# Kernel optimization log

Hardware: AMD Instinct MI355X
Metric: run time of the kernel (lower is better)

Reference implementation:

```python
import jax, jax.numpy as jnp
import numpy as np

Z_CH, TEXT_DIM, HID = 3, 512, 64
B, H, W = 16, 256, 256


def setup_inputs() -> dict:
    key = jax.random.key(0)
    ks = jax.random.split(key, 8)
    z = jax.random.normal(ks[0], (B, Z_CH, H, W), dtype=jnp.float32)
    text_vec = jax.random.normal(ks[1], (B, TEXT_DIM), dtype=jnp.float32)
    # 1x1 conv == per-pixel linear: store weights as [out, in]
    z_proj_w = jax.random.normal(ks[2], (HID, Z_CH), dtype=jnp.float32) * (1.0 / np.sqrt(Z_CH))
    z_proj_b = jnp.zeros((HID,), dtype=jnp.float32)
    text_proj_w = jax.random.normal(ks[3], (HID, TEXT_DIM), dtype=jnp.float32) * (1.0 / np.sqrt(TEXT_DIM))
    text_proj_b = jnp.zeros((HID,), dtype=jnp.float32)
    out_w = jax.random.normal(ks[4], (Z_CH, HID), dtype=jnp.float32) * (1.0 / np.sqrt(HID))
    out_b = jnp.zeros((Z_CH,), dtype=jnp.float32)
    log_gamma = jnp.asarray(1.0 / HID, dtype=jnp.float32)
    alpha = jnp.asarray(0.5, dtype=jnp.float32)
    c = jnp.asarray(1.0, dtype=jnp.float32)
    w = jnp.ones((3,), dtype=jnp.float32)
    return {"z": z, "text_vec": text_vec, "z_proj_w": z_proj_w, "z_proj_b": z_proj_b,
            "text_proj_w": text_proj_w, "text_proj_b": text_proj_b,
            "out_w": out_w, "out_b": out_b,
            "log_gamma": log_gamma, "alpha": alpha, "c": c, "w": w}


def reference(z, text_vec, z_proj_w, z_proj_b, text_proj_w, text_proj_b,
              out_w, out_b, log_gamma, alpha, c, w):
    # z_proj: 1x1 conv -> [B, HID, H, W]
    z_map = jnp.einsum('bchw,oc->bohw', z, z_proj_w) + z_proj_b[None, :, None, None]
    # text_proj: [B, HID]
    t = text_vec @ text_proj_w.T + text_proj_b
    # MultiKernel diagonal: k(z_i, t) per pixel. t_seq broadcasts the same
    # vector to all HW positions, so diag of the full [HW,HW] kernel matrix
    # equals the per-pixel kernel between z_map pixel and t.
    gamma = jnp.exp(log_gamma)
    diff = z_map - t[:, :, None, None]            # [B, HID, H, W]
    dist = jnp.sum(diff * diff, axis=1)            # squared euclidean, [B, H, W]
    k_lin = jnp.einsum('bchw,bc->bhw', z_map, t)   # [B, H, W]
    k_rbf = jnp.exp(-gamma * dist)
    k_poly = (alpha * k_lin + c) ** 2
    k = (w[0] * k_rbf + w[1] * k_lin + w[2] * k_poly) / (jnp.sum(w) + 1e-8)
    weight = k[:, None, :, :]                       # [B, 1, H, W]
    z_fused = z_map * (1.0 + jax.nn.sigmoid(weight))
    out = jnp.einsum('bchw,oc->bohw', z_fused, out_w) + out_b[None, :, None, None]
    return out
```

## Files before the change

kernel.cpp:

```cpp
#include <hip/hip_runtime.h>
#include <math.h>

#define HW_PIX 65536
#define TDIM 512

__device__ __forceinline__ float wred64(float v) {
#pragma unroll
    for (int off = 32; off > 0; off >>= 1) v += __shfl_xor(v, off, 64);
    return v;
}

__global__ __launch_bounds__(256) void fused_kernel(
    const float* __restrict__ z,
    const float* __restrict__ text_vec,
    const float* __restrict__ text_proj_w,
    const float* __restrict__ text_proj_b,
    const float* __restrict__ z_proj_w,
    const float* __restrict__ z_proj_b,
    const float* __restrict__ out_w,
    const float* __restrict__ out_bias,
    const float* __restrict__ log_gamma,
    const float* __restrict__ alpha_p,
    const float* __restrict__ c_p,
    const float* __restrict__ wv,
    float* __restrict__ out)
{
    const int blk = blockIdx.x;
    const int b   = blk >> 6;
    const int tid = threadIdx.x;

    __shared__ float t_sh[64];
    __shared__ float red[27];

    {
        const int o = tid >> 2;
        const int q = tid & 3;
        const float4* tv = (const float4*)(text_vec + (size_t)b * TDIM);
        const float4* wr = (const float4*)(text_proj_w + (size_t)o * TDIM);
        float acc = 0.f;
#pragma unroll 8
        for (int i = q * 32; i < q * 32 + 32; ++i) {
            float4 a = tv[i], w4 = wr[i];
            acc = fmaf(a.x, w4.x, fmaf(a.y, w4.y, fmaf(a.z, w4.z, fmaf(a.w, w4.w, acc))));
        }
        acc += __shfl_xor(acc, 1, 64);
        acc += __shfl_xor(acc, 2, 64);
        if (q == 0) t_sh[o] = acc + text_proj_b[o];
    }
    __syncthreads();

    {
        const int wave = tid >> 6, lane = tid & 63;
        const float t  = t_sh[lane];
        const float w0 = z_proj_w[lane * 3 + 0];
        const float w1 = z_proj_w[lane * 3 + 1];
        const float w2 = z_proj_w[lane * 3 + 2];
        const float zb = z_proj_b[lane];
        const float o0 = out_w[0 * 64 + lane];
        const float o1 = out_w[1 * 64 + lane];
        const float o2 = out_w[2 * 64 + lane];

        float pr[7];
        int n = 7;
        if (wave == 0) {
            pr[0] = w0 * t;  pr[1] = w1 * t;  pr[2] = w2 * t;
            pr[3] = zb * t;  pr[4] = t * t;   pr[5] = w0 * w0; pr[6] = w0 * w1;
        } else if (wave == 1) {
            pr[0] = w0 * w2; pr[1] = w1 * w1; pr[2] = w1 * w2;
            pr[3] = w2 * w2; pr[4] = o0 * w0; pr[5] = o0 * w1; pr[6] = o0 * w2;
        } else if (wave == 2) {
            pr[0] = o1 * w0; pr[1] = o1 * w1; pr[2] = o1 * w2;
            pr[3] = o2 * w0; pr[4] = o2 * w1; pr[5] = o2 * w2; pr[6] = o0 * zb;
        } else {
            pr[0] = o1 * zb; pr[1] = o2 * zb; pr[2] = w0 * zb;
            pr[3] = w1 * zb; pr[4] = w2 * zb; pr[5] = zb * zb; pr[6] = 0.f;
            n = 6;
        }
#pragma unroll
        for (int k = 0; k < 7; ++k) pr[k] = wred64(pr[k]);
        if (lane == 0) {
            const int base = wave * 7;
            for (int k = 0; k < n; ++k) red[base + k] = pr[k];
        }
    }
    __syncthreads();

    const float u0 = red[0], u1 = red[1], u2 = red[2], s = red[3], tn = red[4];
    const float G00 = red[5], G01 = red[6], G02 = red[7];
    const float G11 = red[8], G12 = red[9], G22 = red[10];
    const float M00 = red[11], M01 = red[12], M02 = red[13];
    const float M10 = red[14], M11 = red[15], M12 = red[16];
    const float M20 = red[17], M21 = red[18], M22 = red[19];
    const float v0 = red[20], v1 = red[21], v2 = red[22];
    const float g0 = red[23], g1 = red[24], g2 = red[25], bn = red[26];

    const float gamma = __expf(log_gamma[0]);
    const float alpha = alpha_p[0], cc = c_p[0];
    const float w0 = wv[0], w1 = wv[1], w2 = wv[2];
    const float invw = 1.0f / (w0 + w1 + w2 + 1e-8f);
    const float ob0 = out_bias[0], ob1 = out_bias[1], ob2 = out_bias[2];

    const float e0 = g0 - u0, e1 = g1 - u1, e2 = g2 - u2;
    const float d0 = bn - 2.f * s + tn;

    const int p = ((blk & 63) << 10) + (tid << 2);
    const float* zb = z + (size_t)b * 3 * HW_PIX + p;
    float4 q0 = *(const float4*)(zb);
    float4 q1 = *(const float4*)(zb + HW_PIX);
    float4 q2 = *(const float4*)(zb + 2 * HW_PIX);

    float X[4] = {q0.x, q0.y, q0.z, q0.w};
    float Y[4] = {q1.x, q1.y, q1.z, q1.w};
    float Z[4] = {q2.x, q2.y, q2.z, q2.w};
    float O0[4], O1[4], O2[4];

#pragma unroll
    for (int j = 0; j < 4; ++j) {
        const float x = X[j], y = Y[j], zc = Z[j];
        const float klin = fmaf(x, u0, fmaf(y, u1, fmaf(zc, u2, s)));
        const float quad = x * fmaf(2.f, fmaf(G01, y, G02 * zc), G00 * x)
                         + y * fmaf(2.f, G12 * zc, G11 * y)
                         + G22 * zc * zc;
        const float dist = quad + 2.f * fmaf(e0, x, fmaf(e1, y, e2 * zc)) + d0;
        const float krbf = __expf(-gamma * dist);
        float kp = fmaf(alpha, klin, cc);
        kp = kp * kp;
        const float k = (w0 * krbf + w1 * klin + w2 * kp) * invw;
        const float sig = 1.f / (1.f + __expf(-k));
        const float scale = 1.f + sig;

        const float m0 = fmaf(M00, x, fmaf(M01, y, fmaf(M02, zc, v0)));
        const float m1 = fmaf(M10, x, fmaf(M11, y, fmaf(M12, zc, v1)));
        const float m2 = fmaf(M20, x, fmaf(M21, y, fmaf(M22, zc, v2)));
        O0[j] = fmaf(scale, m0, ob0);
        O1[j] = fmaf(scale, m1, ob1);
        O2[j] = fmaf(scale, m2, ob2);
    }

    float* ob = out + (size_t)b * 3 * HW_PIX + p;
    *(float4*)(ob)              = make_float4(O0[0], O0[1], O0[2], O0[3]);
    *(float4*)(ob + HW_PIX)     = make_float4(O1[0], O1[1], O1[2], O1[3]);
    *(float4*)(ob + 2 * HW_PIX) = make_float4(O2[0], O2[1], O2[2], O2[3]);
}

extern "C" void kernel_launch(void* const* d_in, const int* in_sizes, int n_in,
                              void* d_out, int out_size, void* d_ws, size_t ws_size,
                              hipStream_t stream) {
    const float* z           = (const float*)d_in[0];
    const float* text_vec    = (const float*)d_in[1];
    const float* z_proj_w    = (const float*)d_in[2];
    const float* z_proj_b    = (const float*)d_in[3];
    const float* text_proj_w = (const float*)d_in[4];
    const float* text_proj_b = (const float*)d_in[5];
    const float* out_w       = (const float*)d_in[6];
    const float* out_b       = (const float*)d_in[7];
    const float* log_gamma   = (const float*)d_in[8];
    const float* alpha       = (const float*)d_in[9];
    const float* c           = (const float*)d_in[10];
    const float* w           = (const float*)d_in[11];
    float* out = (float*)d_out;
    (void)d_ws; (void)ws_size; (void)in_sizes; (void)n_in;

    fused_kernel<<<1024, 256, 0, stream>>>(z, text_vec, text_proj_w, text_proj_b,
                                           z_proj_w, z_proj_b, out_w, out_b,
                                           log_gamma, alpha, c, w, out);
}
```

Measured before the change: 115.5 us.

## Split constant precompute into prep kernel and widen streaming kernel to 8 pixels

The per-batch text projection and the weight Gram/product reductions, which every block used to recompute, move into a small 17-block prep kernel that writes the constants to workspace. The main kernel loads those constants as vectors, handles 8 pixels per thread over 512 blocks, and writes its output with nontemporal stores. This removes the redundant 512-wide dot products and block syncs from the streaming kernel. In exchange it adds a second kernel launch and a serial dependency through workspace, and halves the number of blocks.

Result: faster. 94.26 us (-18.4%).

```diff
diff --git a/kernel.cpp b/kernel.cpp
--- a/kernel.cpp
+++ b/kernel.cpp
@@ -3,6 +3,8 @@
 
 #define HW_PIX 65536
 #define TDIM 512
+
+typedef float f4 __attribute__((ext_vector_type(4)));
 
 __device__ __forceinline__ float wred64(float v) {
 #pragma unroll
@@ -10,8 +12,12 @@
     return v;
 }
 
-__global__ __launch_bounds__(256) void fused_kernel(
-    const float* __restrict__ z,
+__device__ __forceinline__ f4 ld4(const float* p) { return *(const f4*)p; }
+__device__ __forceinline__ void st4nt(float* p, f4 v) {
+    __builtin_nontemporal_store(v, (f4*)p);
+}
+
+__global__ __launch_bounds__(256) void prep_kernel(
     const float* __restrict__ text_vec,
     const float* __restrict__ text_proj_w,
     const float* __restrict__ text_proj_b,
@@ -23,16 +29,13 @@
     const float* __restrict__ alpha_p,
     const float* __restrict__ c_p,
     const float* __restrict__ wv,
-    float* __restrict__ out)
+    float* __restrict__ ws)
 {
     const int blk = blockIdx.x;
-    const int b   = blk >> 6;
     const int tid = threadIdx.x;
 
-    __shared__ float t_sh[64];
-    __shared__ float red[27];
-
-    {
+    if (blk < 16) {
+        const int b = blk;
         const int o = tid >> 2;
         const int q = tid & 3;
         const float4* tv = (const float4*)(text_vec + (size_t)b * TDIM);
@@ -45,13 +48,30 @@
         }
         acc += __shfl_xor(acc, 1, 64);
         acc += __shfl_xor(acc, 2, 64);
+
+        __shared__ float t_sh[64];
         if (q == 0) t_sh[o] = acc + text_proj_b[o];
-    }
-    __syncthreads();
-
-    {
+        __syncthreads();
+
+        if (tid < 64) {
+            const float t  = t_sh[tid];
+            const float w0 = z_proj_w[tid * 3 + 0];
+            const float w1 = z_proj_w[tid * 3 + 1];
+            const float w2 = z_proj_w[tid * 3 + 2];
+            const float zb = z_proj_b[tid];
+            float u0 = wred64(w0 * t);
+            float u1 = wred64(w1 * t);
+            float u2 = wred64(w2 * t);
+            float s  = wred64(zb * t);
+            float tn = wred64(t * t);
+            if (tid == 0) {
+                float* pb = ws + b * 8;
+                pb[0] = u0; pb[1] = u1; pb[2] = u2; pb[3] = s;
+                pb[4] = fmaf(-2.f, s, tn);
+            }
+        }
+    } else {
         const int wave = tid >> 6, lane = tid & 63;
-        const float t  = t_sh[lane];
         const float w0 = z_proj_w[lane * 3 + 0];
         const float w1 = z_proj_w[lane * 3 + 1];
         const float w2 = z_proj_w[lane * 3 + 2];
@@ -59,73 +79,90 @@
         const float o0 = out_w[0 * 64 + lane];
         const float o1 = out_w[1 * 64 + lane];
         const float o2 = out_w[2 * 64 + lane];
-
-        float pr[7];
-        int n = 7;
+        float* c = ws + 128;
         if (wave == 0) {
-            pr[0] = w0 * t;  pr[1] = w1 * t;  pr[2] = w2 * t;
-            pr[3] = zb * t;  pr[4] = t * t;   pr[5] = w0 * w0; pr[6] = w0 * w1;
+            float r0 = wred64(w0 * w0), r1 = wred64(w0 * w1), r2 = wred64(w0 * w2);
+            float r3 = wred64(w1 * w1), r4 = wred64(w1 * w2), r5 = wred64(w2 * w2);
+            if (lane == 0) { c[0]=r0; c[1]=r1; c[2]=r2; c[3]=r3; c[4]=r4; c[5]=r5; }
         } else if (wave == 1) {
-            pr[0] = w0 * w2; pr[1] = w1 * w1; pr[2] = w1 * w2;
-            pr[3] = w2 * w2; pr[4] = o0 * w0; pr[5] = o0 * w1; pr[6] = o0 * w2;
+            float r0 = wred64(o0 * w0), r1 = wred64(o0 * w1), r2 = wred64(o0 * w2);
+            float r3 = wred64(o1 * w0), r4 = wred64(o1 * w1), r5 = wred64(o1 * w2);
+            if (lane == 0) { c[6]=r0; c[7]=r1; c[8]=r2; c[9]=r3; c[10]=r4; c[11]=r5; }
         } else if (wave == 2) {
-            pr[0] = o1 * w0; pr[1] = o1 * w1; pr[2] = o1 * w2;
-            pr[3] = o2 * w0; pr[4] = o2 * w1; pr[5] = o2 * w2; pr[6] = o0 * zb;
+            float r0 = wred64(o2 * w0), r1 = wred64(o2 * w1), r2 = wred64(o2 * w2);
+            float r3 = wred64(zb * zb), r4 = wred64(o0 * zb), r5 = wred64(o1 * zb);
+            if (lane == 0) { c[12]=r0; c[13]=r1; c[14]=r2; c[15]=r3; c[16]=r4; c[17]=r5; }
         } else {
-            pr[0] = o1 * zb; pr[1] = o2 * zb; pr[2] = w0 * zb;
-            pr[3] = w1 * zb; pr[4] = w2 * zb; pr[5] = zb * zb; pr[6] = 0.f;
-            n = 6;
-        }
-#pragma unroll
-        for (int k = 0; k < 7; ++k) pr[k] = wred64(pr[k]);
-        if (lane == 0) {
-            const int base = wave * 7;
-            for (int k = 0; k < n; ++k) red[base + k] = pr[k];
+            float r0 = wred64(o2 * zb), r1 = wred64(w0 * zb);
+            float r2 = wred64(w1 * zb), r3 = wred64(w2 * zb);
+            if (lane == 0) {
+                c[18] = r0;
+                c[20] = r1; c[21] = r2; c[22] = r3;
+                c[19] = -__expf(log_gamma[0]);
+                c[23] = alpha_p[0];
+                c[24] = c_p[0];
+                float a = wv[0], bb = wv[1], d = wv[2];
+                float inv = 1.f / (a + bb + d + 1e-8f);
+                c[25] = a * inv; c[26] = bb * inv; c[27] = d * inv;
+                c[28] = out_bias[0]; c[29] = out_bias[1]; c[30] = out_bias[2];
+                c[31] = 0.f;
+            }
         }
     }
-    __syncthreads();
-
-    const float u0 = red[0], u1 = red[1], u2 = red[2], s = red[3], tn = red[4];
-    const float G00 = red[5], G01 = red[6], G02 = red[7];
-    const float G11 = red[8], G12 = red[9], G22 = red[10];
-    const float M00 = red[11], M01 = red[12], M02 = red[13];
-    const float M10 = red[14], M11 = red[15], M12 = red[16];
-    const float M20 = red[17], M21 = red[18], M22 = red[19];
-    const float v0 = red[20], v1 = red[21], v2 = red[22];
-    const float g0 = red[23], g1 = red[24], g2 = red[25], bn = red[26];
-
-    const float gamma = __expf(log_gamma[0]);
-    const float alpha = alpha_p[0], cc = c_p[0];
-    const float w0 = wv[0], w1 = wv[1], w2 = wv[2];
-    const float invw = 1.0f / (w0 + w1 + w2 + 1e-8f);
-    const float ob0 = out_bias[0], ob1 = out_bias[1], ob2 = out_bias[2];
-
+}
+
+__global__ __launch_bounds__(256) void fuse_kernel(
+    const float* __restrict__ z,
+    const float* __restrict__ ws,
+    float* __restrict__ out)
+{
+    const int blk = blockIdx.x;
+    const int b   = blk >> 5;
+    const int p   = ((blk & 31) << 11) + (threadIdx.x << 3);
+
+    const f4* C4 = (const f4*)(ws + 128);
+    const f4 f0 = C4[0], f1 = C4[1], f2 = C4[2], f3 = C4[3];
+    const f4 f4v = C4[4], f5 = C4[5], f6 = C4[6], f7 = C4[7];
+    const float G00=f0[0], G01=f0[1], G02=f0[2], G11=f0[3];
+    const float G12=f1[0], G22=f1[1], M00=f1[2], M01=f1[3];
+    const float M02=f2[0], M10=f2[1], M11=f2[2], M12=f2[3];
+    const float M20=f3[0], M21=f3[1], M22=f3[2], bn =f3[3];
+    const float v0=f4v[0], v1=f4v[1], v2=f4v[2], ngamma=f4v[3];
+    const float g0=f5[0], g1=f5[1], g2=f5[2], alpha=f5[3];
+    const float cc=f6[0], W0=f6[1], W1=f6[2], W2=f6[3];
+    const float ob0=f7[0], ob1=f7[1], ob2=f7[2];
+
+    const f4* pb4 = (const f4*)(ws + b * 8);
+    const f4 pbA = pb4[0], pbB = pb4[1];
+    const float u0=pbA[0], u1=pbA[1], u2=pbA[2], s=pbA[3];
+    const float d0 = bn + pbB[0];
     const float e0 = g0 - u0, e1 = g1 - u1, e2 = g2 - u2;
-    const float d0 = bn - 2.f * s + tn;
-
-    const int p = ((blk & 63) << 10) + (tid << 2);
+
     const float* zb = z + (size_t)b * 3 * HW_PIX + p;
-    float4 q0 = *(const float4*)(zb);
-    float4 q1 = *(const float4*)(zb + HW_PIX);
-    float4 q2 = *(const float4*)(zb + 2 * HW_PIX);
-
-    float X[4] = {q0.x, q0.y, q0.z, q0.w};
-    float Y[4] = {q1.x, q1.y, q1.z, q1.w};
-    float Z[4] = {q2.x, q2.y, q2.z, q2.w};
-    float O0[4], O1[4], O2[4];
-
+    f4 a0 = ld4(zb),            a1 = ld4(zb + 4);
+    f4 b0 = ld4(zb + HW_PIX),   b1 = ld4(zb + HW_PIX + 4);
+    f4 c0 = ld4(zb + 2*HW_PIX), c1 = ld4(zb + 2*HW_PIX + 4);
+
+    float X[8], Y[8], Z[8], O0[8], O1[8], O2[8];
 #pragma unroll
     for (int j = 0; j < 4; ++j) {
+        X[j] = a0[j]; X[j+4] = a1[j];
+        Y[j] = b0[j]; Y[j+4] = b1[j];
+        Z[j] = c0[j]; Z[j+4] = c1[j];
+    }
+
+#pragma unroll
+    for (int j = 0; j < 8; ++j) {
         const float x = X[j], y = Y[j], zc = Z[j];
         const float klin = fmaf(x, u0, fmaf(y, u1, fmaf(zc, u2, s)));
         const float quad = x * fmaf(2.f, fmaf(G01, y, G02 * zc), G00 * x)
                          + y * fmaf(2.f, G12 * zc, G11 * y)
                          + G22 * zc * zc;
         const float dist = quad + 2.f * fmaf(e0, x, fmaf(e1, y, e2 * zc)) + d0;
-        const float krbf = __expf(-gamma * dist);
+        const float krbf = __expf(ngamma * dist);
         float kp = fmaf(alpha, klin, cc);
         kp = kp * kp;
-        const float k = (w0 * krbf + w1 * klin + w2 * kp) * invw;
+        const float k = fmaf(W0, krbf, fmaf(W1, klin, W2 * kp));
         const float sig = 1.f / (1.f + __expf(-k));
         const float scale = 1.f + sig;
 
@@ -138,9 +175,13 @@
     }
 
     float* ob = out + (size_t)b * 3 * HW_PIX + p;
-    *(float4*)(ob)              = make_float4(O0[0], O0[1], O0[2], O0[3]);
-    *(float4*)(ob + HW_PIX)     = make_float4(O1[0], O1[1], O1[2], O1[3]);
-    *(float4*)(ob + 2 * HW_PIX) = make_float4(O2[0], O2[1], O2[2], O2[3]);
+    f4 r;
+    r[0]=O0[0]; r[1]=O0[1]; r[2]=O0[2]; r[3]=O0[3]; st4nt(ob, r);
+    r[0]=O0[4]; r[1]=O0[5]; r[2]=O0[6]; r[3]=O0[7]; st4nt(ob + 4, r);
+    r[0]=O1[0]; r[1]=O1[1]; r[2]=O1[2]; r[3]=O1[3]; st4nt(ob + HW_PIX, r);
+    r[0]=O1[4]; r[1]=O1[5]; r[2]=O1[6]; r[3]=O1[7]; st4nt(ob + HW_PIX + 4, r);
+    r[0]=O2[0]; r[1]=O2[1]; r[2]=O2[2]; r[3]=O2[3]; st4nt(ob + 2*HW_PIX, r);
+    r[0]=O2[4]; r[1]=O2[5]; r[2]=O2[6]; r[3]=O2[7]; st4nt(ob + 2*HW_PIX + 4, r);
 }
 
 extern "C" void kernel_launch(void* const* d_in, const int* in_sizes, int n_in,
@@ -159,9 +200,11 @@
     const float* c           = (const float*)d_in[10];
     const float* w           = (const float*)d_in[11];
     float* out = (float*)d_out;
-    (void)d_ws; (void)ws_size; (void)in_sizes; (void)n_in;
-
-    fused_kernel<<<1024, 256, 0, stream>>>(z, text_vec, text_proj_w, text_proj_b,
-                                           z_proj_w, z_proj_b, out_w, out_b,
-                                           log_gamma, alpha, c, w, out);
-}
+    float* ws  = (float*)d_ws;
+    (void)in_sizes; (void)n_in; (void)out_size; (void)ws_size;
+
+    prep_kernel<<<17, 256, 0, stream>>>(text_vec, text_proj_w, text_proj_b,
+                                        z_proj_w, z_proj_b, out_w, out_b,
+                                        log_gamma, alpha, c, w, ws);
+    fuse_kernel<<<512, 256, 0, stream>>>(z, ws, out);
+}
```
